# Kernel optimization log

Hardware: AMD Instinct MI355X
Metric: run time of the kernel (lower is better)

The kernel has to match this reference:

```python
import jax, jax.numpy as jnp
import numpy as np

N_G = 1024
H, W = 192, 256
FX, FY, CX, CY = 220.0, 220.0, 128.0, 96.0
NEAR, FAR = 0.01, 10.0
MARGIN = 0.1
ALPHA_THR = 1e-5
C0 = 0.28209479177387814
C1 = 0.4886025119029199
C2 = (1.0925484305920792, -1.0925484305920792, 0.31539156525252005, -1.0925484305920792, 0.5462742152960396)
C3 = (-0.5900435899266435, 2.890611442640554, -0.4570457994644658, 0.3731763325901154, -0.4570457994644658, 1.445305721320277, -0.5900435899266435)


def setup_inputs() -> dict:
    key = jax.random.key(0)
    k = jax.random.split(key, 6)
    xy = jax.random.uniform(k[0], (N_G, 2), minval=-1.5, maxval=1.5)
    z = jax.random.uniform(k[1], (N_G, 1), minval=0.5, maxval=6.0)
    positions = jnp.concatenate([xy, z], axis=1)
    rotations = jax.random.normal(k[2], (N_G, 4))
    scales = jnp.log(jax.random.uniform(k[3], (N_G, 3), minval=0.02, maxval=0.1))  # log-scale, as in module
    opacity = jax.random.uniform(k[4], (N_G, 1), minval=0.1, maxval=0.9)
    sh_coeffs = 0.3 * jax.random.normal(k[5], (N_G, 16, 3))
    T_WC = jnp.eye(4, dtype=jnp.float32)
    return {"positions": positions, "rotations": rotations, "scales": scales,
            "opacity": opacity, "sh_coeffs": sh_coeffs, "T_WC": T_WC}


def _quat_to_rot(q):
    q = q / (jnp.linalg.norm(q, axis=1, keepdims=True) + 1e-12)
    w, x, y, z = q[:, 0], q[:, 1], q[:, 2], q[:, 3]
    R = jnp.stack([
        1 - 2 * (y * y + z * z), 2 * (x * y - w * z), 2 * (x * z + w * y),
        2 * (x * y + w * z), 1 - 2 * (x * x + z * z), 2 * (y * z - w * x),
        2 * (x * z - w * y), 2 * (y * z + w * x), 1 - 2 * (x * x + y * y)], axis=1)
    return R.reshape(-1, 3, 3)


def _eval_sh(sh, d):
    # sh: [N,16,3] degree-3 SH, d: [N,3] unit view dirs (standard 3DGS real SH)
    x, y, z = d[:, 0:1], d[:, 1:2], d[:, 2:3]
    c = C0 * sh[:, 0] - C1 * y * sh[:, 1] + C1 * z * sh[:, 2] - C1 * x * sh[:, 3]
    xx, yy, zz = x * x, y * y, z * z
    xy, yz, xz = x * y, y * z, x * z
    c = c + C2[0] * xy * sh[:, 4] + C2[1] * yz * sh[:, 5] + C2[2] * (2 * zz - xx - yy) * sh[:, 6] \
          + C2[3] * xz * sh[:, 7] + C2[4] * (xx - yy) * sh[:, 8]
    c = c + C3[0] * y * (3 * xx - yy) * sh[:, 9] + C3[1] * xy * z * sh[:, 10] \
          + C3[2] * y * (4 * zz - xx - yy) * sh[:, 11] + C3[3] * z * (2 * zz - 3 * xx - 3 * yy) * sh[:, 12] \
          + C3[4] * x * (4 * zz - xx - yy) * sh[:, 13] + C3[5] * z * (xx - yy) * sh[:, 14] \
          + C3[6] * x * (xx - 3 * yy) * sh[:, 15]
    return jnp.clip(c + 0.5, 0.0, 1.0)


def _forward(positions, rotations, scales, opacity, sh_coeffs, T_WC):
    n = positions.shape[0]
    pts_h = jnp.concatenate([positions, jnp.ones((n, 1), positions.dtype)], axis=1)
    pc = (pts_h @ T_WC.T)[:, :3]  # world -> camera
    xs_c, ys_c, z = pc[:, 0], pc[:, 1], pc[:, 2]
    az = jnp.abs(z)
    x_fac = max(CX / FX, (W - CX) / FX)
    y_fac = max(CY / FY, (H - CY) / FY)
    valid = (az > NEAR) & (az < FAR) \
        & (jnp.abs(xs_c) < az * x_fac * (1 + MARGIN)) \
        & (jnp.abs(ys_c) < az * y_fac * (1 + MARGIN))
    zs = jnp.where(jnp.abs(z) < 1e-8, 1e-8, z)
    u = FX * xs_c / zs + CX
    v = FY * ys_c / zs + CY
    # 3D covariance Sigma = (R S)(R S)^T, then 2D via perspective Jacobian J Sigma J^T
    R = _quat_to_rot(rotations)
    S = jnp.exp(scales)  # scales stored in log space
    M = R * S[:, None, :]
    cov3d = jnp.einsum('nij,nkj->nik', M, M)
    zero = jnp.zeros_like(zs)
    J = jnp.stack([
        jnp.stack([FX / zs, zero, -FX * xs_c / (zs * zs)], axis=1),
        jnp.stack([zero, FY / zs, -FY * ys_c / (zs * zs)], axis=1)], axis=1)
    cov2d = jnp.einsum('nij,njk,nlk->nil', J, cov3d, J)
    a = cov2d[:, 0, 0] + 0.3  # low-pass dilation as in 3DGS
    b = cov2d[:, 0, 1]
    c = cov2d[:, 1, 1] + 0.3
    det = jnp.maximum(a * c - b * b, 1e-12)
    A, B, Cc = c / det, -b / det, a / det  # conic (inverse covariance)
    # frustum culling as mask: culled gaussians contribute zero opacity
    op = opacity[:, 0] * valid.astype(positions.dtype)
    dirs = pc / (jnp.linalg.norm(pc, axis=1, keepdims=True) + 1e-12)
    colors = _eval_sh(sh_coeffs, dirs)  # [N,3]
    # depth sort DESCENDING (as in module) -> back-to-front painter compositing
    order = jnp.argsort(-z)
    u, v, A, B, Cc, op, zd, colors = (t[order] for t in (u, v, A, B, Cc, op, z, colors))
    # dense per-pixel evaluation  [P, N]
    px = jnp.arange(W, dtype=positions.dtype) + 0.5
    py = jnp.arange(H, dtype=positions.dtype) + 0.5
    gx, gy = jnp.meshgrid(px, py)  # [H, W]
    gx, gy = gx.reshape(-1, 1), gy.reshape(-1, 1)
    dx = gx - u[None, :]
    dy = gy - v[None, :]
    power = -0.5 * (A[None, :] * dx * dx + Cc[None, :] * dy * dy) - B[None, :] * dx * dy
    alpha = jnp.minimum(0.99, op[None, :] * jnp.exp(jnp.minimum(power, 0.0)))
    alpha = jnp.where(alpha < ALPHA_THR, 0.0, alpha)
    # back-to-front: C = sum_i c_i a_i prod_{j>i} (1-a_j)  (exclusive suffix product)
    one_m = 1.0 - alpha
    cp = jnp.cumprod(one_m[:, ::-1], axis=1)
    T = jnp.concatenate([jnp.ones((alpha.shape[0], 1), alpha.dtype), cp[:, :-1]], axis=1)[:, ::-1]
    w = alpha * T
    rgb = (w @ colors).reshape(H, W, 3)
    depth = (w @ zd).reshape(H, W, 1)
    return rgb, depth


def reference(positions, rotations, scales, opacity, sh_coeffs, T_WC):
    return _forward(positions, rotations, scales, opacity, sh_coeffs, T_WC)
```

## Files before the change

kernel.cpp:

```cpp
#include <hip/hip_runtime.h>
#include <hip/hip_bf16.h>
#include <hip/hip_fp16.h>

#define NG 1024
#define IMW 256
#define IMH 192
#define NPIX (IMW*IMH)
#define FXc 220.0f
#define FYc 220.0f
#define CXc 128.0f
#define CYc 96.0f
#define NEARc 0.01f
#define FARc 10.0f
#define ALPHA_THRc 1e-5f

#define SH_C0 0.28209479177387814f
#define SH_C1 0.4886025119029199f
#define SH_C2_0 1.0925484305920792f
#define SH_C2_1 (-1.0925484305920792f)
#define SH_C2_2 0.31539156525252005f
#define SH_C2_3 (-1.0925484305920792f)
#define SH_C2_4 0.5462742152960396f
#define SH_C3_0 (-0.5900435899266435f)
#define SH_C3_1 2.890611442640554f
#define SH_C3_2 (-0.4570457994644658f)
#define SH_C3_3 0.3731763325901154f
#define SH_C3_4 (-0.4570457994644658f)
#define SH_C3_5 1.445305721320277f
#define SH_C3_6 (-0.5900435899266435f)


__global__ __launch_bounds__(64)
void gs_prep(const float* __restrict__ pos, const float* __restrict__ rot,
             const float* __restrict__ scl, const float* __restrict__ opac,
             const float* __restrict__ sh,  const float* __restrict__ Twc,
             float4* __restrict__ g0, float4* __restrict__ g1,
             float2* __restrict__ g2) {
    int i = blockIdx.x * 64 + threadIdx.x;
    if (i >= NG) return;

    float p0 = pos[i*3+0], p1 = pos[i*3+1], p2 = pos[i*3+2];
    float xc = Twc[0]*p0 + Twc[1]*p1 + Twc[2]*p2  + Twc[3];
    float yc = Twc[4]*p0 + Twc[5]*p1 + Twc[6]*p2  + Twc[7];
    float zc = Twc[8]*p0 + Twc[9]*p1 + Twc[10]*p2 + Twc[11];

    float az = fabsf(zc);
    const float xfac = fmaxf(CXc/FXc, (IMW - CXc)/FXc) * 1.1f;
    const float yfac = fmaxf(CYc/FYc, (IMH - CYc)/FYc) * 1.1f;
    bool valid = (az > NEARc) && (az < FARc) &&
                 (fabsf(xc) < az * xfac) && (fabsf(yc) < az * yfac);

    float zs = (az < 1e-8f) ? 1e-8f : zc;
    float iz = 1.0f / zs;
    float u = FXc * xc * iz + CXc;
    float v = FYc * yc * iz + CYc;

    float qw = rot[i*4+0], qx = rot[i*4+1], qy = rot[i*4+2], qz = rot[i*4+3];
    float qn = sqrtf(qw*qw + qx*qx + qy*qy + qz*qz) + 1e-12f;
    float inq = 1.0f / qn;
    qw *= inq; qx *= inq; qy *= inq; qz *= inq;
    float R00 = 1.0f - 2.0f*(qy*qy + qz*qz);
    float R01 = 2.0f*(qx*qy - qw*qz);
    float R02 = 2.0f*(qx*qz + qw*qy);
    float R10 = 2.0f*(qx*qy + qw*qz);
    float R11 = 1.0f - 2.0f*(qx*qx + qz*qz);
    float R12 = 2.0f*(qy*qz - qw*qx);
    float R20 = 2.0f*(qx*qz - qw*qy);
    float R21 = 2.0f*(qy*qz + qw*qx);
    float R22 = 1.0f - 2.0f*(qx*qx + qy*qy);

    float s0 = expf(scl[i*3+0]);
    float s1 = expf(scl[i*3+1]);
    float s2 = expf(scl[i*3+2]);
    float M00 = R00*s0, M01 = R01*s1, M02 = R02*s2;
    float M10 = R10*s0, M11 = R11*s1, M12 = R12*s2;
    float M20 = R20*s0, M21 = R21*s1, M22 = R22*s2;

    float S00 = M00*M00 + M01*M01 + M02*M02;
    float S01 = M00*M10 + M01*M11 + M02*M12;
    float S02 = M00*M20 + M01*M21 + M02*M22;
    float S11 = M10*M10 + M11*M11 + M12*M12;
    float S12 = M10*M20 + M11*M21 + M12*M22;
    float S22 = M20*M20 + M21*M21 + M22*M22;

    float j00 = FXc * iz,  j02 = -FXc * xc * iz * iz;
    float j11 = FYc * iz,  j12 = -FYc * yc * iz * iz;
    float c00 = j00*j00*S00 + 2.0f*j00*j02*S02 + j02*j02*S22 + 0.3f;
    float c01 = j00*j11*S01 + j00*j12*S02 + j02*j11*S12 + j02*j12*S22;
    float c11 = j11*j11*S11 + 2.0f*j11*j12*S12 + j12*j12*S22 + 0.3f;
    float det = fmaxf(c00*c11 - c01*c01, 1e-12f);
    float idet = 1.0f / det;
    float Ai = c11 * idet;
    float Bi = -c01 * idet;
    float Ci = c00 * idet;

    float op = valid ? opac[i] : 0.0f;

    float Q = fmaxf(2.0f * logf(fmaxf(op, 1e-20f) * 1e5f), 0.0f);
    float rx = valid ? (sqrtf(Q * c00) + 1e-3f) : -1e9f;
    float ry = valid ? (sqrtf(Q * c11) + 1e-3f) : -1e9f;

    float pn = sqrtf(xc*xc + yc*yc + zc*zc) + 1e-12f;
    float ipn = 1.0f / pn;
    float dx = xc*ipn, dy = yc*ipn, dz = zc*ipn;
    float xx = dx*dx, yy = dy*dy, zz = dz*dz;
    float xy = dx*dy, yz = dy*dz, xz = dx*dz;

    const float* s = sh + i*48;
    float col[3];
#pragma unroll
    for (int ch = 0; ch < 3; ++ch) {
        float c = SH_C0*s[0+ch] - SH_C1*dy*s[3+ch] + SH_C1*dz*s[6+ch] - SH_C1*dx*s[9+ch];
        c += SH_C2_0*xy*s[12+ch] + SH_C2_1*yz*s[15+ch] + SH_C2_2*(2.0f*zz-xx-yy)*s[18+ch]
           + SH_C2_3*xz*s[21+ch] + SH_C2_4*(xx-yy)*s[24+ch];
        c += SH_C3_0*dy*(3.0f*xx-yy)*s[27+ch] + SH_C3_1*xy*dz*s[30+ch]
           + SH_C3_2*dy*(4.0f*zz-xx-yy)*s[33+ch] + SH_C3_3*dz*(2.0f*zz-3.0f*xx-3.0f*yy)*s[36+ch]
           + SH_C3_4*dx*(4.0f*zz-xx-yy)*s[39+ch] + SH_C3_5*dz*(xx-yy)*s[42+ch]
           + SH_C3_6*dx*(xx-3.0f*yy)*s[45+ch];
        col[ch] = fminf(fmaxf(c + 0.5f, 0.0f), 1.0f);
    }

    __half2 rg = __floats2half2_rn(col[0], col[1]);
    __half2 bz = __floats2half2_rn(col[2], zc);

    g0[i] = make_float4(u, v, Ai, Bi);
    g1[i] = make_float4(Ci, op, __uint_as_float(*(unsigned int*)&rg),
                                __uint_as_float(*(unsigned int*)&bz));
    g2[i] = make_float2(rx, ry);
}

__global__ __launch_bounds__(64)
void gs_tile(const float4* __restrict__ g0, const float4* __restrict__ g1,
             const float2* __restrict__ g2, float* __restrict__ out) {
    __shared__ float4 sv0[NG], sv1[NG];
    __shared__ unsigned long long key[NG];
    __shared__ unsigned short ord[NG];
    __shared__ int scnt;

    int t = threadIdx.x;
    if (t == 0) scnt = 0;
    __syncthreads();

    float tx0 = (float)(blockIdx.x * 8) + 0.5f;
    float tx1 = tx0 + 7.0f;
    float ty0 = (float)(blockIdx.y * 8) + 0.5f;
    float ty1 = ty0 + 7.0f;

#pragma unroll 4
    for (int p = 0; p < 16; ++p) {
        int i = p * 64 + t;
        float4 a0 = g0[i];
        float2 a2 = g2[i];
        bool pass = (a0.x + a2.x >= tx0) && (a0.x - a2.x <= tx1) &&
                    (a0.y + a2.y >= ty0) && (a0.y - a2.y <= ty1);
        if (pass) {
            int pos = atomicAdd(&scnt, 1);
            sv0[pos] = a0;
            float4 a1 = g1[i];
            sv1[pos] = a1;
            unsigned int zb = __float_as_uint(__high2float(*(__half2*)&a1.w));
            zb = (zb & 0x80000000u) ? ~zb : (zb | 0x80000000u);
            key[pos] = ((unsigned long long)zb << 32) | (unsigned int)(NG - 1 - i);
        }
    }
    __syncthreads();
    int M = scnt;

    for (int s = t; s < M; s += 64) {
        unsigned long long ks = key[s];
        int rank = 0;
        for (int j = 0; j < M; ++j)
            rank += (key[j] < ks) ? 1 : 0;
        ord[rank] = (unsigned short)s;
    }
    __syncthreads();

    float px = tx0 + (float)(t & 7);
    float py = ty0 + (float)(t >> 3);
    float T = 1.0f;
    float cr = 0.0f, cg = 0.0f, cb = 0.0f, cd = 0.0f;

#pragma unroll 2
    for (int j = 0; j < M; ++j) {
        int slot = ord[j];
        float4 a0 = sv0[slot];
        float4 a1 = sv1[slot];
        float dx = px - a0.x;
        float dy = py - a0.y;
        float pw = -0.5f * (a0.z * dx * dx + a1.x * dy * dy) - a0.w * dx * dy;
        pw = fminf(pw, 0.0f);
        float alpha = fminf(0.99f, a1.y * __expf(pw));
        float aeff = (alpha >= ALPHA_THRc) ? alpha : 0.0f;
        float w = aeff * T;
        float2 rg = __half22float2(*(__half2*)&a1.z);
        float2 bz = __half22float2(*(__half2*)&a1.w);
        cr += w * rg.x;
        cg += w * rg.y;
        cb += w * bz.x;
        cd += w * bz.y;
        T *= 1.0f - aeff;
        if (__all(T < 1e-4f)) break;
    }

    int x = blockIdx.x * 8 + (t & 7);
    int y = blockIdx.y * 8 + (t >> 3);
    int idx = y * IMW + x;
    out[idx*3 + 0] = cr;
    out[idx*3 + 1] = cg;
    out[idx*3 + 2] = cb;
    out[NPIX*3 + idx] = cd;
}

extern "C" void kernel_launch(void* const* d_in, const int* in_sizes, int n_in,
                              void* d_out, int out_size, void* d_ws, size_t ws_size,
                              hipStream_t stream) {
    const float* pos  = (const float*)d_in[0];
    const float* rot  = (const float*)d_in[1];
    const float* scl  = (const float*)d_in[2];
    const float* opac = (const float*)d_in[3];
    const float* sh   = (const float*)d_in[4];
    const float* Twc  = (const float*)d_in[5];
    float* out = (float*)d_out;

    char* ws = (char*)d_ws;
    float4* g0 = (float4*)ws;
    float4* g1 = (float4*)(ws + 16384);
    float2* g2 = (float2*)(ws + 32768);

    gs_prep<<<dim3(NG/64), dim3(64), 0, stream>>>(pos, rot, scl, opac, sh, Twc,
                                                  g0, g1, g2);
    gs_tile<<<dim3(IMW/8, IMH/8), dim3(64), 0, stream>>>(g0, g1, g2, out);
}
```

Before: 29.66 us.

## Sort gaussians globally by depth once in prep instead of per tile

Moves the depth sort from every 8x8 tile block into the prep kernel. Each of 16 blocks recomputes camera-space z for all 1024 gaussians and ranks its 64 by counting, with 256 threads splitting the comparisons, then scatters the prepared data in sorted order. The tile kernel then streams the sorted arrays in chunks of 64, compacts passing gaussians with a ballot into shared memory, and composites each chunk with an early-exit check between chunks. This removes the per-tile O(M^2) rank sort and the large shared buffers, at the cost of redundant z computation in prep, extra barriers per chunk, and exact-key tie handling for invalid gaussians.

New measurement: 26.32 us. 11.3% less time.

```diff
diff --git a/kernel.cpp b/kernel.cpp
--- a/kernel.cpp
+++ b/kernel.cpp
@@ -30,180 +30,202 @@
 #define SH_C3_6 (-0.5900435899266435f)
 
 
-__global__ __launch_bounds__(64)
-void gs_prep(const float* __restrict__ pos, const float* __restrict__ rot,
-             const float* __restrict__ scl, const float* __restrict__ opac,
-             const float* __restrict__ sh,  const float* __restrict__ Twc,
-             float4* __restrict__ g0, float4* __restrict__ g1,
-             float2* __restrict__ g2) {
-    int i = blockIdx.x * 64 + threadIdx.x;
-    if (i >= NG) return;
-
-    float p0 = pos[i*3+0], p1 = pos[i*3+1], p2 = pos[i*3+2];
-    float xc = Twc[0]*p0 + Twc[1]*p1 + Twc[2]*p2  + Twc[3];
-    float yc = Twc[4]*p0 + Twc[5]*p1 + Twc[6]*p2  + Twc[7];
-    float zc = Twc[8]*p0 + Twc[9]*p1 + Twc[10]*p2 + Twc[11];
-
-    float az = fabsf(zc);
+__global__ __launch_bounds__(256)
+void gs_prepsort(const float* __restrict__ pos, const float* __restrict__ rot,
+                 const float* __restrict__ scl, const float* __restrict__ opac,
+                 const float* __restrict__ sh,  const float* __restrict__ Twc,
+                 float4* __restrict__ g0, float4* __restrict__ g1,
+                 float2* __restrict__ g2) {
+    __shared__ unsigned long long keys[NG];
+    __shared__ int pr[256];
+
+    int t = threadIdx.x;
+    int b = blockIdx.x;
+
+    float T0 = Twc[0],  T1 = Twc[1],  T2 = Twc[2],  T3 = Twc[3];
+    float T4 = Twc[4],  T5 = Twc[5],  T6 = Twc[6],  T7 = Twc[7];
+    float T8 = Twc[8],  T9 = Twc[9],  T10 = Twc[10], T11 = Twc[11];
+
     const float xfac = fmaxf(CXc/FXc, (IMW - CXc)/FXc) * 1.1f;
     const float yfac = fmaxf(CYc/FYc, (IMH - CYc)/FYc) * 1.1f;
-    bool valid = (az > NEARc) && (az < FARc) &&
-                 (fabsf(xc) < az * xfac) && (fabsf(yc) < az * yfac);
-
-    float zs = (az < 1e-8f) ? 1e-8f : zc;
-    float iz = 1.0f / zs;
-    float u = FXc * xc * iz + CXc;
-    float v = FYc * yc * iz + CYc;
-
-    float qw = rot[i*4+0], qx = rot[i*4+1], qy = rot[i*4+2], qz = rot[i*4+3];
-    float qn = sqrtf(qw*qw + qx*qx + qy*qy + qz*qz) + 1e-12f;
-    float inq = 1.0f / qn;
-    qw *= inq; qx *= inq; qy *= inq; qz *= inq;
-    float R00 = 1.0f - 2.0f*(qy*qy + qz*qz);
-    float R01 = 2.0f*(qx*qy - qw*qz);
-    float R02 = 2.0f*(qx*qz + qw*qy);
-    float R10 = 2.0f*(qx*qy + qw*qz);
-    float R11 = 1.0f - 2.0f*(qx*qx + qz*qz);
-    float R12 = 2.0f*(qy*qz - qw*qx);
-    float R20 = 2.0f*(qx*qz - qw*qy);
-    float R21 = 2.0f*(qy*qz + qw*qx);
-    float R22 = 1.0f - 2.0f*(qx*qx + qy*qy);
-
-    float s0 = expf(scl[i*3+0]);
-    float s1 = expf(scl[i*3+1]);
-    float s2 = expf(scl[i*3+2]);
-    float M00 = R00*s0, M01 = R01*s1, M02 = R02*s2;
-    float M10 = R10*s0, M11 = R11*s1, M12 = R12*s2;
-    float M20 = R20*s0, M21 = R21*s1, M22 = R22*s2;
-
-    float S00 = M00*M00 + M01*M01 + M02*M02;
-    float S01 = M00*M10 + M01*M11 + M02*M12;
-    float S02 = M00*M20 + M01*M21 + M02*M22;
-    float S11 = M10*M10 + M11*M11 + M12*M12;
-    float S12 = M10*M20 + M11*M21 + M12*M22;
-    float S22 = M20*M20 + M21*M21 + M22*M22;
-
-    float j00 = FXc * iz,  j02 = -FXc * xc * iz * iz;
-    float j11 = FYc * iz,  j12 = -FYc * yc * iz * iz;
-    float c00 = j00*j00*S00 + 2.0f*j00*j02*S02 + j02*j02*S22 + 0.3f;
-    float c01 = j00*j11*S01 + j00*j12*S02 + j02*j11*S12 + j02*j12*S22;
-    float c11 = j11*j11*S11 + 2.0f*j11*j12*S12 + j12*j12*S22 + 0.3f;
-    float det = fmaxf(c00*c11 - c01*c01, 1e-12f);
-    float idet = 1.0f / det;
-    float Ai = c11 * idet;
-    float Bi = -c01 * idet;
-    float Ci = c00 * idet;
-
-    float op = valid ? opac[i] : 0.0f;
-
-    float Q = fmaxf(2.0f * logf(fmaxf(op, 1e-20f) * 1e5f), 0.0f);
-    float rx = valid ? (sqrtf(Q * c00) + 1e-3f) : -1e9f;
-    float ry = valid ? (sqrtf(Q * c11) + 1e-3f) : -1e9f;
-
-    float pn = sqrtf(xc*xc + yc*yc + zc*zc) + 1e-12f;
-    float ipn = 1.0f / pn;
-    float dx = xc*ipn, dy = yc*ipn, dz = zc*ipn;
-    float xx = dx*dx, yy = dy*dy, zz = dz*dz;
-    float xy = dx*dy, yz = dy*dz, xz = dx*dz;
-
-    const float* s = sh + i*48;
-    float col[3];
+
 #pragma unroll
-    for (int ch = 0; ch < 3; ++ch) {
-        float c = SH_C0*s[0+ch] - SH_C1*dy*s[3+ch] + SH_C1*dz*s[6+ch] - SH_C1*dx*s[9+ch];
-        c += SH_C2_0*xy*s[12+ch] + SH_C2_1*yz*s[15+ch] + SH_C2_2*(2.0f*zz-xx-yy)*s[18+ch]
-           + SH_C2_3*xz*s[21+ch] + SH_C2_4*(xx-yy)*s[24+ch];
-        c += SH_C3_0*dy*(3.0f*xx-yy)*s[27+ch] + SH_C3_1*xy*dz*s[30+ch]
-           + SH_C3_2*dy*(4.0f*zz-xx-yy)*s[33+ch] + SH_C3_3*dz*(2.0f*zz-3.0f*xx-3.0f*yy)*s[36+ch]
-           + SH_C3_4*dx*(4.0f*zz-xx-yy)*s[39+ch] + SH_C3_5*dz*(xx-yy)*s[42+ch]
-           + SH_C3_6*dx*(xx-3.0f*yy)*s[45+ch];
-        col[ch] = fminf(fmaxf(c + 0.5f, 0.0f), 1.0f);
+    for (int p = 0; p < 4; ++p) {
+        int i = p * 256 + t;
+        float p0 = pos[i*3+0], p1 = pos[i*3+1], p2 = pos[i*3+2];
+        float xc = T0*p0 + T1*p1 + T2*p2  + T3;
+        float yc = T4*p0 + T5*p1 + T6*p2  + T7;
+        float zc = T8*p0 + T9*p1 + T10*p2 + T11;
+        float az = fabsf(zc);
+        bool valid = (az > NEARc) && (az < FARc) &&
+                     (fabsf(xc) < az * xfac) && (fabsf(yc) < az * yfac);
+        bool keep = valid && (opac[i] > 0.0f);
+        unsigned int zb = __float_as_uint(zc);
+        zb = (zb & 0x80000000u) ? ~zb : (zb | 0x80000000u);
+        unsigned int lo = (unsigned int)(NG - 1 - i);
+        keys[i] = keep ? (((unsigned long long)zb << 32) | lo)
+                       : ((0xFFFFFFFFull << 32) | lo);
     }
-
-    __half2 rg = __floats2half2_rn(col[0], col[1]);
-    __half2 bz = __floats2half2_rn(col[2], zc);
-
-    g0[i] = make_float4(u, v, Ai, Bi);
-    g1[i] = make_float4(Ci, op, __uint_as_float(*(unsigned int*)&rg),
-                                __uint_as_float(*(unsigned int*)&bz));
-    g2[i] = make_float2(rx, ry);
+    __syncthreads();
+
+    int l = t & 63, seg = t >> 6;
+    int gi = b * 64 + l;
+    unsigned long long kg = keys[gi];
+    int partial = 0;
+    int jb = seg * 256;
+#pragma unroll 4
+    for (int j = jb; j < jb + 256; ++j)
+        partial += (keys[j] < kg) ? 1 : 0;
+    pr[t] = partial;
+    __syncthreads();
+
+    if (t < 64) {
+        int i = b * 64 + t;
+        int rank = pr[t] + pr[t+64] + pr[t+128] + pr[t+192];
+
+        float p0 = pos[i*3+0], p1 = pos[i*3+1], p2 = pos[i*3+2];
+        float xc = T0*p0 + T1*p1 + T2*p2  + T3;
+        float yc = T4*p0 + T5*p1 + T6*p2  + T7;
+        float zc = T8*p0 + T9*p1 + T10*p2 + T11;
+        float az = fabsf(zc);
+        bool valid = (az > NEARc) && (az < FARc) &&
+                     (fabsf(xc) < az * xfac) && (fabsf(yc) < az * yfac);
+
+        float zs = (az < 1e-8f) ? 1e-8f : zc;
+        float iz = 1.0f / zs;
+        float u = FXc * xc * iz + CXc;
+        float v = FYc * yc * iz + CYc;
+
+        float qw = rot[i*4+0], qx = rot[i*4+1], qy = rot[i*4+2], qz = rot[i*4+3];
+        float qn = sqrtf(qw*qw + qx*qx + qy*qy + qz*qz) + 1e-12f;
+        float inq = 1.0f / qn;
+        qw *= inq; qx *= inq; qy *= inq; qz *= inq;
+        float R00 = 1.0f - 2.0f*(qy*qy + qz*qz);
+        float R01 = 2.0f*(qx*qy - qw*qz);
+        float R02 = 2.0f*(qx*qz + qw*qy);
+        float R10 = 2.0f*(qx*qy + qw*qz);
+        float R11 = 1.0f - 2.0f*(qx*qx + qz*qz);
+        float R12 = 2.0f*(qy*qz - qw*qx);
+        float R20 = 2.0f*(qx*qz - qw*qy);
+        float R21 = 2.0f*(qy*qz + qw*qx);
+        float R22 = 1.0f - 2.0f*(qx*qx + qy*qy);
+
+        float s0 = expf(scl[i*3+0]);
+        float s1 = expf(scl[i*3+1]);
+        float s2 = expf(scl[i*3+2]);
+        float M00 = R00*s0, M01 = R01*s1, M02 = R02*s2;
+        float M10 = R10*s0, M11 = R11*s1, M12 = R12*s2;
+        float M20 = R20*s0, M21 = R21*s1, M22 = R22*s2;
+
+        float S00 = M00*M00 + M01*M01 + M02*M02;
+        float S01 = M00*M10 + M01*M11 + M02*M12;
+        float S02 = M00*M20 + M01*M21 + M02*M22;
+        float S11 = M10*M10 + M11*M11 + M12*M12;
+        float S12 = M10*M20 + M11*M21 + M12*M22;
+        float S22 = M20*M20 + M21*M21 + M22*M22;
+
+        float j00 = FXc * iz,  j02 = -FXc * xc * iz * iz;
+        float j11 = FYc * iz,  j12 = -FYc * yc * iz * iz;
+        float c00 = j00*j00*S00 + 2.0f*j00*j02*S02 + j02*j02*S22 + 0.3f;
+        float c01 = j00*j11*S01 + j00*j12*S02 + j02*j11*S12 + j02*j12*S22;
+        float c11 = j11*j11*S11 + 2.0f*j11*j12*S12 + j12*j12*S22 + 0.3f;
+        float det = fmaxf(c00*c11 - c01*c01, 1e-12f);
+        float idet = 1.0f / det;
+        float Ai = c11 * idet;
+        float Bi = -c01 * idet;
+        float Ci = c00 * idet;
+
+        float op = valid ? opac[i] : 0.0f;
+
+        float Q = fmaxf(2.0f * logf(fmaxf(op, 1e-20f) * 1e5f), 0.0f);
+        float rx = valid ? (sqrtf(Q * c00) + 1e-3f) : -1e9f;
+        float ry = valid ? (sqrtf(Q * c11) + 1e-3f) : -1e9f;
+
+        float pn = sqrtf(xc*xc + yc*yc + zc*zc) + 1e-12f;
+        float ipn = 1.0f / pn;
+        float dx = xc*ipn, dy = yc*ipn, dz = zc*ipn;
+        float xx = dx*dx, yy = dy*dy, zz = dz*dz;
+        float xy = dx*dy, yz = dy*dz, xz = dx*dz;
+
+        const float* s = sh + i*48;
+        float col[3];
+#pragma unroll
+        for (int ch = 0; ch < 3; ++ch) {
+            float c = SH_C0*s[0+ch] - SH_C1*dy*s[3+ch] + SH_C1*dz*s[6+ch] - SH_C1*dx*s[9+ch];
+            c += SH_C2_0*xy*s[12+ch] + SH_C2_1*yz*s[15+ch] + SH_C2_2*(2.0f*zz-xx-yy)*s[18+ch]
+               + SH_C2_3*xz*s[21+ch] + SH_C2_4*(xx-yy)*s[24+ch];
+            c += SH_C3_0*dy*(3.0f*xx-yy)*s[27+ch] + SH_C3_1*xy*dz*s[30+ch]
+               + SH_C3_2*dy*(4.0f*zz-xx-yy)*s[33+ch] + SH_C3_3*dz*(2.0f*zz-3.0f*xx-3.0f*yy)*s[36+ch]
+               + SH_C3_4*dx*(4.0f*zz-xx-yy)*s[39+ch] + SH_C3_5*dz*(xx-yy)*s[42+ch]
+               + SH_C3_6*dx*(xx-3.0f*yy)*s[45+ch];
+            col[ch] = fminf(fmaxf(c + 0.5f, 0.0f), 1.0f);
+        }
+
+        __half2 rg = __floats2half2_rn(col[0], col[1]);
+        __half2 bz = __floats2half2_rn(col[2], zc);
+
+        g0[rank] = make_float4(u, v, Ai, Bi);
+        g1[rank] = make_float4(Ci, op, __uint_as_float(*(unsigned int*)&rg),
+                                       __uint_as_float(*(unsigned int*)&bz));
+        g2[rank] = make_float2(rx, ry);
+    }
 }
 
 __global__ __launch_bounds__(64)
 void gs_tile(const float4* __restrict__ g0, const float4* __restrict__ g1,
              const float2* __restrict__ g2, float* __restrict__ out) {
-    __shared__ float4 sv0[NG], sv1[NG];
-    __shared__ unsigned long long key[NG];
-    __shared__ unsigned short ord[NG];
-    __shared__ int scnt;
-
-    int t = threadIdx.x;
-    if (t == 0) scnt = 0;
-    __syncthreads();
-
+    __shared__ float4 ls0[64], ls1[64];
+
+    int lane = threadIdx.x;
     float tx0 = (float)(blockIdx.x * 8) + 0.5f;
     float tx1 = tx0 + 7.0f;
     float ty0 = (float)(blockIdx.y * 8) + 0.5f;
     float ty1 = ty0 + 7.0f;
 
-#pragma unroll 4
-    for (int p = 0; p < 16; ++p) {
-        int i = p * 64 + t;
-        float4 a0 = g0[i];
-        float2 a2 = g2[i];
-        bool pass = (a0.x + a2.x >= tx0) && (a0.x - a2.x <= tx1) &&
-                    (a0.y + a2.y >= ty0) && (a0.y - a2.y <= ty1);
-        if (pass) {
-            int pos = atomicAdd(&scnt, 1);
-            sv0[pos] = a0;
-            float4 a1 = g1[i];
-            sv1[pos] = a1;
-            unsigned int zb = __float_as_uint(__high2float(*(__half2*)&a1.w));
-            zb = (zb & 0x80000000u) ? ~zb : (zb | 0x80000000u);
-            key[pos] = ((unsigned long long)zb << 32) | (unsigned int)(NG - 1 - i);
-        }
-    }
-    __syncthreads();
-    int M = scnt;
-
-    for (int s = t; s < M; s += 64) {
-        unsigned long long ks = key[s];
-        int rank = 0;
-        for (int j = 0; j < M; ++j)
-            rank += (key[j] < ks) ? 1 : 0;
-        ord[rank] = (unsigned short)s;
-    }
-    __syncthreads();
-
-    float px = tx0 + (float)(t & 7);
-    float py = ty0 + (float)(t >> 3);
+    float px = tx0 + (float)(lane & 7);
+    float py = ty0 + (float)(lane >> 3);
     float T = 1.0f;
     float cr = 0.0f, cg = 0.0f, cb = 0.0f, cd = 0.0f;
 
-#pragma unroll 2
-    for (int j = 0; j < M; ++j) {
-        int slot = ord[j];
-        float4 a0 = sv0[slot];
-        float4 a1 = sv1[slot];
-        float dx = px - a0.x;
-        float dy = py - a0.y;
-        float pw = -0.5f * (a0.z * dx * dx + a1.x * dy * dy) - a0.w * dx * dy;
-        pw = fminf(pw, 0.0f);
-        float alpha = fminf(0.99f, a1.y * __expf(pw));
-        float aeff = (alpha >= ALPHA_THRc) ? alpha : 0.0f;
-        float w = aeff * T;
-        float2 rg = __half22float2(*(__half2*)&a1.z);
-        float2 bz = __half22float2(*(__half2*)&a1.w);
-        cr += w * rg.x;
-        cg += w * rg.y;
-        cb += w * bz.x;
-        cd += w * bz.y;
-        T *= 1.0f - aeff;
+    for (int c = 0; c < NG/64; ++c) {
+        int i = c * 64 + lane;
+        float4 a0 = g0[i];
+        float2 rr = g2[i];
+        bool pass = (a0.x + rr.x >= tx0) && (a0.x - rr.x <= tx1) &&
+                    (a0.y + rr.y >= ty0) && (a0.y - rr.y <= ty1);
+        unsigned long long m = __ballot(pass);
+        if (m == 0ull) continue;
+        if (pass) {
+            int slot = __popcll(m & ((1ull << lane) - 1ull));
+            ls0[slot] = a0;
+            ls1[slot] = g1[i];
+        }
+        __syncthreads();
+        int mt = __popcll(m);
+        for (int j = 0; j < mt; ++j) {
+            float4 b0 = ls0[j];
+            float4 b1 = ls1[j];
+            float dx = px - b0.x;
+            float dy = py - b0.y;
+            float pw = -0.5f * (b0.z * dx * dx + b1.x * dy * dy) - b0.w * dx * dy;
+            pw = fminf(pw, 0.0f);
+            float alpha = fminf(0.99f, b1.y * __expf(pw));
+            float aeff = (alpha >= ALPHA_THRc) ? alpha : 0.0f;
+            float w = aeff * T;
+            float2 rg = __half22float2(*(__half2*)&b1.z);
+            float2 bz = __half22float2(*(__half2*)&b1.w);
+            cr += w * rg.x;
+            cg += w * rg.y;
+            cb += w * bz.x;
+            cd += w * bz.y;
+            T *= 1.0f - aeff;
+        }
+        __syncthreads();
         if (__all(T < 1e-4f)) break;
     }
 
-    int x = blockIdx.x * 8 + (t & 7);
-    int y = blockIdx.y * 8 + (t >> 3);
+    int x = blockIdx.x * 8 + (lane & 7);
+    int y = blockIdx.y * 8 + (lane >> 3);
     int idx = y * IMW + x;
     out[idx*3 + 0] = cr;
     out[idx*3 + 1] = cg;
@@ -227,7 +249,7 @@
     float4* g1 = (float4*)(ws + 16384);
     float2* g2 = (float2*)(ws + 32768);
 
-    gs_prep<<<dim3(NG/64), dim3(64), 0, stream>>>(pos, rot, scl, opac, sh, Twc,
-                                                  g0, g1, g2);
+    gs_prepsort<<<dim3(NG/64), dim3(256), 0, stream>>>(pos, rot, scl, opac, sh,
+                                                       Twc, g0, g1, g2);
     gs_tile<<<dim3(IMW/8, IMH/8), dim3(64), 0, stream>>>(g0, g1, g2, out);
 }
```
